# Kernel optimization log

Measured on AMD Instinct MI355X. Metric: run time of the kernel, lower is better.

The kernel has to match this reference:

```python
import jax, jax.numpy as jnp
import numpy as np

B, N, C, H, W = 16, 10, 128, 48, 48

def setup_inputs() -> dict:
    key = jax.random.key(0)
    k0, k1 = jax.random.split(key, 2)
    x = jax.random.normal(k0, (B, N, C, H, W), dtype=jnp.float32)
    # trainable interpolation params, initialized to 0.5 as in the torch module
    pos_dec = jnp.full((N,), 0.5, dtype=jnp.float32)
    length_dec = jnp.full((N,), 0.5, dtype=jnp.float32)
    # 1x1 conv == channel-mixing matmul over N*C channels
    NC = N * C
    conv_w = jax.random.normal(k1, (NC, NC), dtype=jnp.float32) * (1.0 / np.sqrt(NC))
    conv_b = jnp.zeros((NC,), dtype=jnp.float32)
    return {"x": x, "pos_dec": pos_dec, "length_dec": length_dec,
            "conv_w": conv_w, "conv_b": conv_b}


def reference(x, pos_dec, length_dec, conv_w, conv_b):
    b, n, c, h, w = x.shape
    d = c * h * w
    q = x.reshape(b, n, d)          # proj_query (B,N,CHW)
    k = q                           # proj_key has the same flattened features
    # bi_interpolate with pos_int=i, length_int=1 reduces in closed form to:
    #   s0 = (1-pd)*K[i]   + pd*K[i+1]                      (key_short row)
    #   s1 = ld*((1-pd)*K[i+1] + pd*K[i+2])                 (zero-padded short mixed with key_long)
    # where indices wrap mod N (key was concatenated with itself).
    idx = jnp.arange(n)
    k1_ = k[:, (idx + 1) % n]       # (B,N,D)
    k2_ = k[:, (idx + 2) % n]
    pd = pos_dec[None, :, None]
    ld = length_dec[None, :, None]
    s0 = (1.0 - pd) * k + pd * k1_
    s1 = ld * ((1.0 - pd) * k1_ + pd * k2_)
    S = jnp.stack([s0, s1], axis=2)                 # (B,N,2,D) interpolated keys per group
    logits = jnp.einsum('bnd,bnkd->bnk', q, S)      # per-group 2-way attention scores
    attn = jax.nn.softmax(logits, axis=-1)          # softmax over the 2 searched keys
    out = jnp.einsum('bnk,bnkd->bnd', attn, S)      # (B,N,D)
    feat = out.reshape(b, n * c, h, w)
    conv = jnp.einsum('oc,bchw->bohw', conv_w, feat) + conv_b[None, :, None, None]
    return conv + x.reshape(b, n * c, h, w)
```

## Files before the change

kernel.cpp:

```cpp
#include <hip/hip_runtime.h>
#include <hip/hip_bf16.h>

#define BB 16
#define NN 10
#define CC 128
#define HWD 2304
#define DD (CC*HWD)
#define NC (NN*CC)

#define CH2 72
#define CHUNK2 4096

#define BM 256
#define BN 128
#define BK 32
#define TK (NC/BK)

typedef __bf16 bf16x8 __attribute__((ext_vector_type(8)));
typedef float  f32x4  __attribute__((ext_vector_type(4)));

#define FEAT_BYTES ((size_t)BB*HWD*NC*2)
#define WB_BYTES   ((size_t)NC*NC*2)
#define PART_FLOATS (BB*NN*CH2*3)

__device__ __forceinline__ ushort f2bf(float f) {
    __hip_bfloat16 h = __float2bfloat16(f);
    return *reinterpret_cast<ushort*>(&h);
}

__device__ __forceinline__ void gload_lds16(const ushort* g, ushort* l) {
    __builtin_amdgcn_global_load_lds(
        (const __attribute__((address_space(1))) void*)(const void*)g,
        (__attribute__((address_space(3))) void*)(void*)l,
        16, 0, 0);
}

__global__ __launch_bounds__(256) void k_dots(const float* __restrict__ x,
                                              float* __restrict__ part) {
    int blk = blockIdx.x;
    int ch = blk % CH2;
    int b  = blk / CH2;
    const float* base = x + (size_t)b*NN*DD + (size_t)ch*CHUNK2;
    int t = threadIdx.x;

    float4 cur[4], nxt[4], inc[4];
    #pragma unroll
    for (int i = 0; i < 4; ++i) cur[i] = *(const float4*)(base + (size_t)0*DD + i*1024 + t*4);
    #pragma unroll
    for (int i = 0; i < 4; ++i) nxt[i] = *(const float4*)(base + (size_t)1*DD + i*1024 + t*4);

    __shared__ float red[4][3];
    int w = t >> 6, l = t & 63;

    for (int n = 0; n < NN; ++n) {
        int n2 = (n + 2) % NN;
        #pragma unroll
        for (int i = 0; i < 4; ++i) inc[i] = *(const float4*)(base + (size_t)n2*DD + i*1024 + t*4);

        float s0 = 0.f, s1 = 0.f, s2 = 0.f;
        #pragma unroll
        for (int i = 0; i < 4; ++i) {
            s0 += cur[i].x*cur[i].x + cur[i].y*cur[i].y + cur[i].z*cur[i].z + cur[i].w*cur[i].w;
            s1 += cur[i].x*nxt[i].x + cur[i].y*nxt[i].y + cur[i].z*nxt[i].z + cur[i].w*nxt[i].w;
            s2 += cur[i].x*inc[i].x + cur[i].y*inc[i].y + cur[i].z*inc[i].z + cur[i].w*inc[i].w;
        }
        for (int o = 32; o > 0; o >>= 1) {
            s0 += __shfl_down(s0, o);
            s1 += __shfl_down(s1, o);
            s2 += __shfl_down(s2, o);
        }
        if (l == 0) { red[w][0] = s0; red[w][1] = s1; red[w][2] = s2; }
        __syncthreads();
        if (t == 0) {
            float r0 = 0.f, r1 = 0.f, r2 = 0.f;
            #pragma unroll
            for (int i = 0; i < 4; ++i) { r0 += red[i][0]; r1 += red[i][1]; r2 += red[i][2]; }
            float* o = part + ((size_t)(b*NN + n)*CH2 + ch)*3;
            o[0] = r0; o[1] = r1; o[2] = r2;
        }
        __syncthreads();
        #pragma unroll
        for (int i = 0; i < 4; ++i) { cur[i] = nxt[i]; nxt[i] = inc[i]; }
    }
}

__global__ void k_coef(const float* __restrict__ part,
                       const float* __restrict__ pos_dec,
                       const float* __restrict__ len_dec,
                       float* __restrict__ coef) {
    int bn = threadIdx.x;
    if (bn >= BB*NN) return;
    int n = bn % NN;
    float d0 = 0.f, d1 = 0.f, d2 = 0.f;
    const float* p = part + (size_t)bn*CH2*3;
    for (int i = 0; i < CH2; ++i) { d0 += p[i*3]; d1 += p[i*3+1]; d2 += p[i*3+2]; }
    float pd = pos_dec[n], ld = len_dec[n];
    float l0 = (1.f - pd)*d0 + pd*d1;
    float l1 = ld*((1.f - pd)*d1 + pd*d2);
    float m  = fmaxf(l0, l1);
    float e0 = expf(l0 - m), e1 = expf(l1 - m);
    float inv = 1.f/(e0 + e1);
    float a0 = e0*inv, a1 = e1*inv;
    coef[bn*3+0] = a0*(1.f - pd);
    coef[bn*3+1] = a0*pd + a1*ld*(1.f - pd);
    coef[bn*3+2] = a1*ld*pd;
}

__global__ __launch_bounds__(256) void k_wconv(const float* __restrict__ w,
                                               ushort* __restrict__ wb) {
    int i = blockIdx.x*blockDim.x + threadIdx.x;
    size_t idx = (size_t)i*4;
    if (idx >= (size_t)NC*NC) return;
    float4 a = *(const float4*)(w + idx);
    ushort4 o;
    o.x = f2bf(a.x); o.y = f2bf(a.y); o.z = f2bf(a.z); o.w = f2bf(a.w);
    *(ushort4*)(wb + idx) = o;
}

__global__ __launch_bounds__(256) void k_feat(const float* __restrict__ x,
                                              const float* __restrict__ coef,
                                              ushort* __restrict__ featT) {
    __shared__ float tile[32*129];
    int hwt = blockIdx.x;
    int b   = blockIdx.y;
    int t = threadIdx.x;
    int hw0 = hwt*32;
    const float* xb = x + (size_t)b*NN*DD;

    int c_[4], ch_[4];
    size_t off_[4];
    #pragma unroll
    for (int i = 0; i < 4; ++i) {
        int s = i*256 + t;
        c_[i] = s >> 3; ch_[i] = s & 7;
        off_[i] = (size_t)c_[i]*HWD + hw0 + ch_[i]*4;
    }

    float4 s0[4], s1[4], s2[4], s3[4];
    #pragma unroll
    for (int i = 0; i < 4; ++i) s0[i] = *(const float4*)(xb + (size_t)0*DD + off_[i]);
    #pragma unroll
    for (int i = 0; i < 4; ++i) s1[i] = *(const float4*)(xb + (size_t)1*DD + off_[i]);
    #pragma unroll
    for (int i = 0; i < 4; ++i) s2[i] = *(const float4*)(xb + (size_t)2*DD + off_[i]);

    for (int n = 0; n < NN; ++n) {
        int n3 = (n + 3) % NN;
        #pragma unroll
        for (int i = 0; i < 4; ++i) s3[i] = *(const float4*)(xb + (size_t)n3*DD + off_[i]);

        int bn = b*NN + n;
        float c0 = coef[bn*3+0], c1 = coef[bn*3+1], c2 = coef[bn*3+2];

        #pragma unroll
        for (int i = 0; i < 4; ++i) {
            int hwb = ch_[i]*4, cc = c_[i];
            tile[(hwb+0)*129 + cc] = c0*s0[i].x + c1*s1[i].x + c2*s2[i].x;
            tile[(hwb+1)*129 + cc] = c0*s0[i].y + c1*s1[i].y + c2*s2[i].y;
            tile[(hwb+2)*129 + cc] = c0*s0[i].z + c1*s1[i].z + c2*s2[i].z;
            tile[(hwb+3)*129 + cc] = c0*s0[i].w + c1*s1[i].w + c2*s2[i].w;
        }
        __syncthreads();

        int hwl = t >> 4;
        int cc0 = (t & 15) * 8;
        #pragma unroll
        for (int p = 0; p < 2; ++p) {
            int hw = p*16 + hwl;
            const float* src = &tile[hw*129 + cc0];
            union { ushort us[8]; uint4 v; } pk;
            #pragma unroll
            for (int j = 0; j < 8; ++j) pk.us[j] = f2bf(src[j]);
            ushort* dst = featT + (size_t)b*HWD*NC + (size_t)(hw0 + hw)*NC + n*CC + cc0;
            *(uint4*)dst = pk.v;
        }
        __syncthreads();
        #pragma unroll
        for (int i = 0; i < 4; ++i) { s0[i] = s1[i]; s1[i] = s2[i]; s2[i] = s3[i]; }
    }
}

__global__ __launch_bounds__(512, 4) void k_gemm(const ushort* __restrict__ Wb,
                                                 const ushort* __restrict__ featT,
                                                 const float* __restrict__ bias,
                                                 const float* __restrict__ x,
                                                 float* __restrict__ out) {
    __shared__ ushort As[2][BM*BK];
    __shared__ ushort Bs[2][BN*BK];

    int bid = blockIdx.x;
    int wkid = (bid & 7) * 180 + (bid >> 3);
    int b    = wkid / 90;
    int rem  = wkid % 90;
    int hwt  = rem / 5;
    int ot   = rem % 5;
    int o0 = ot*BM, hw0 = hwt*BN;

    int t = threadIdx.x;
    int l = t & 63;
    int w = t >> 6;
    int wr = w >> 1, wc = w & 1;

    const ushort* Ag = Wb + (size_t)o0*NC;
    const ushort* Bg = featT + (size_t)b*HWD*NC + (size_t)hw0*NC;

    int r0 = t >> 2, c0 = t & 3;
    size_t g0 = (size_t)r0*NC + (size_t)((c0 ^ ((r0 >> 1) & 3)) * 8);

#define STAGE(buf_, kt_) do { \
    size_t k0_ = (size_t)(kt_)*BK; \
    ushort* da_ = &As[buf_][0]; \
    ushort* db_ = &Bs[buf_][0]; \
    gload_lds16(Ag + g0 + k0_,                  da_ + t*8); \
    gload_lds16(Ag + g0 + (size_t)128*NC + k0_, da_ + (512 + t)*8); \
    gload_lds16(Bg + g0 + k0_,                  db_ + t*8); \
} while (0)

    int fr = l & 15;
    int fc = l >> 4;

    f32x4 acc[4][4] = {};

    STAGE(0, 0);
    __syncthreads();

    for (int kt = 0; kt < TK; ++kt) {
        int buf = kt & 1;
        if (kt + 1 < TK) STAGE(buf ^ 1, kt + 1);
        __builtin_amdgcn_sched_barrier(0);

        const ushort* as = &As[buf][0];
        const ushort* bs = &Bs[buf][0];

        bf16x8 afr[4], bfr[4];
        #pragma unroll
        for (int m = 0; m < 4; ++m) {
            int row = wr*64 + m*16 + fr;
            afr[m] = *(const bf16x8*)&as[row*BK + ((fc ^ ((row >> 1) & 3))*8)];
        }
        #pragma unroll
        for (int n = 0; n < 4; ++n) {
            int row = wc*64 + n*16 + fr;
            bfr[n] = *(const bf16x8*)&bs[row*BK + ((fc ^ ((row >> 1) & 3))*8)];
        }
        #pragma unroll
        for (int m = 0; m < 4; ++m)
            #pragma unroll
            for (int n = 0; n < 4; ++n)
                acc[m][n] = __builtin_amdgcn_mfma_f32_16x16x32_bf16(afr[m], bfr[n], acc[m][n], 0, 0, 0);

        __syncthreads();
    }
#undef STAGE

    #pragma unroll
    for (int m = 0; m < 4; ++m) {
        int ro_base = o0 + wr*64 + m*16 + ((l >> 4) << 2);
        #pragma unroll
        for (int n = 0; n < 4; ++n) {
            int col = hw0 + wc*64 + n*16 + (l & 15);
            #pragma unroll
            for (int r = 0; r < 4; ++r) {
                int ro = ro_base + r;
                size_t idx = (size_t)b*NC*HWD + (size_t)ro*HWD + col;
                out[idx] = acc[m][n][r] + bias[ro] + x[idx];
            }
        }
    }
}

extern "C" void kernel_launch(void* const* d_in, const int* in_sizes, int n_in,
                              void* d_out, int out_size, void* d_ws, size_t ws_size,
                              hipStream_t stream) {
    const float* x       = (const float*)d_in[0];
    const float* pos_dec = (const float*)d_in[1];
    const float* len_dec = (const float*)d_in[2];
    const float* conv_w  = (const float*)d_in[3];
    const float* conv_b  = (const float*)d_in[4];
    float* out = (float*)d_out;

    char* ws = (char*)d_ws;
    ushort* featT = (ushort*)ws;
    ushort* wb    = (ushort*)(ws + FEAT_BYTES);
    float*  part  = (float*)(ws + FEAT_BYTES + WB_BYTES);
    float*  coef  = part + PART_FLOATS;

    k_dots <<<dim3(BB*CH2), 256, 0, stream>>>(x, part);
    k_coef <<<dim3(1), 256, 0, stream>>>(part, pos_dec, len_dec, coef);
    k_wconv<<<dim3(1600), 256, 0, stream>>>(conv_w, wb);
    k_feat <<<dim3(72, BB), 256, 0, stream>>>(x, coef, featT);
    k_gemm <<<dim3(1440), 512, 0, stream>>>(wb, featT, conv_b, x, out);
}
```

Baseline: 305.8 us.

## Enlarge GEMM tile to 256x256x64 with finely interleaved LDS/MFMA pipeline

The GEMM tile grows from 256x128 with K=32 to 256x256 with K=64, which halves the block count. Each K step is split into four 32-wide sub-tiles whose global-to-LDS loads are issued between MFMA phases, using explicit barriers, waitcnt and setprio. The larger tile raises operand reuse and cuts global and LDS traffic per FLOP. In exchange it holds more accumulator registers and runs at lower occupancy (launch bounds 2), with only 720 blocks to fill the CUs.

Measured after the change: 300.2 us. Within noise of the previous version (-1.8%).

```diff
diff --git a/kernel.cpp b/kernel.cpp
--- a/kernel.cpp
+++ b/kernel.cpp
@@ -12,8 +12,8 @@
 #define CHUNK2 4096
 
 #define BM 256
-#define BN 128
-#define BK 32
+#define BN 256
+#define BK 64
 #define TK (NC/BK)
 
 typedef __bf16 bf16x8 __attribute__((ext_vector_type(8)));
@@ -180,82 +180,170 @@
     }
 }
 
-__global__ __launch_bounds__(512, 4) void k_gemm(const ushort* __restrict__ Wb,
+#define BAR()   __builtin_amdgcn_s_barrier()
+#define SB()    __builtin_amdgcn_sched_barrier(0)
+#define LGKM0() asm volatile("s_waitcnt lgkmcnt(0)" ::: "memory")
+#define VM(N)   asm volatile("s_waitcnt vmcnt(" #N ")" ::: "memory")
+
+__global__ __launch_bounds__(512, 2) void k_gemm(const ushort* __restrict__ Wb,
                                                  const ushort* __restrict__ featT,
                                                  const float* __restrict__ bias,
                                                  const float* __restrict__ x,
                                                  float* __restrict__ out) {
-    __shared__ ushort As[2][BM*BK];
-    __shared__ ushort Bs[2][BN*BK];
+    __shared__ ushort L[2][4][BM*32];
 
     int bid = blockIdx.x;
-    int wkid = (bid & 7) * 180 + (bid >> 3);
-    int b    = wkid / 90;
-    int rem  = wkid % 90;
-    int hwt  = rem / 5;
-    int ot   = rem % 5;
+    int wkid = (bid & 7) * 90 + (bid >> 3);
+    int b   = wkid / 45;
+    int r45 = wkid % 45;
+    int hwt = r45 / 5;
+    int ot  = r45 % 5;
     int o0 = ot*BM, hw0 = hwt*BN;
 
     int t = threadIdx.x;
     int l = t & 63;
     int w = t >> 6;
-    int wr = w >> 1, wc = w & 1;
+    int wr = w >> 2, wc = w & 3;
 
     const ushort* Ag = Wb + (size_t)o0*NC;
     const ushort* Bg = featT + (size_t)b*HWD*NC + (size_t)hw0*NC;
 
     int r0 = t >> 2, c0 = t & 3;
     size_t g0 = (size_t)r0*NC + (size_t)((c0 ^ ((r0 >> 1) & 3)) * 8);
-
-#define STAGE(buf_, kt_) do { \
-    size_t k0_ = (size_t)(kt_)*BK; \
-    ushort* da_ = &As[buf_][0]; \
-    ushort* db_ = &Bs[buf_][0]; \
-    gload_lds16(Ag + g0 + k0_,                  da_ + t*8); \
-    gload_lds16(Ag + g0 + (size_t)128*NC + k0_, da_ + (512 + t)*8); \
-    gload_lds16(Bg + g0 + k0_,                  db_ + t*8); \
-} while (0)
+    size_t g1 = g0 + (size_t)128*NC;
+
+#define STAGE(nb_, reg_, gp_) do { \
+    gload_lds16((gp_) + g0, &L[nb_][reg_][t*8]); \
+    gload_lds16((gp_) + g1, &L[nb_][reg_][(512 + t)*8]); } while (0)
 
     int fr = l & 15;
-    int fc = l >> 4;
-
-    f32x4 acc[4][4] = {};
-
-    STAGE(0, 0);
-    __syncthreads();
-
-    for (int kt = 0; kt < TK; ++kt) {
-        int buf = kt & 1;
-        if (kt + 1 < TK) STAGE(buf ^ 1, kt + 1);
-        __builtin_amdgcn_sched_barrier(0);
-
-        const ushort* as = &As[buf][0];
-        const ushort* bs = &Bs[buf][0];
-
-        bf16x8 afr[4], bfr[4];
-        #pragma unroll
-        for (int m = 0; m < 4; ++m) {
-            int row = wr*64 + m*16 + fr;
-            afr[m] = *(const bf16x8*)&as[row*BK + ((fc ^ ((row >> 1) & 3))*8)];
-        }
-        #pragma unroll
-        for (int n = 0; n < 4; ++n) {
-            int row = wc*64 + n*16 + fr;
-            bfr[n] = *(const bf16x8*)&bs[row*BK + ((fc ^ ((row >> 1) & 3))*8)];
-        }
-        #pragma unroll
-        for (int m = 0; m < 4; ++m)
-            #pragma unroll
-            for (int n = 0; n < 4; ++n)
-                acc[m][n] = __builtin_amdgcn_mfma_f32_16x16x32_bf16(afr[m], bfr[n], acc[m][n], 0, 0, 0);
-
-        __syncthreads();
+    int kc = ((l >> 4) ^ ((l >> 1) & 3)) * 8;
+    int rowA = (wr*128 + fr)*32 + kc;
+    int rowB = (wc*64  + fr)*32 + kc;
+
+    f32x4 acc[8][4] = {};
+    bf16x8 af[8], bfA, bfB;
+
+    STAGE(0, 0, Ag);
+    STAGE(0, 2, Bg);
+    STAGE(0, 1, Ag + 32);
+    STAGE(0, 3, Bg + 32);
+    VM(4);
+    BAR(); SB();
+
+    for (int kt = 0; kt < TK - 1; ++kt) {
+        int buf = kt & 1, nbuf = buf ^ 1;
+        const ushort* A0 = &L[buf][0][0];
+        const ushort* A1 = &L[buf][1][0];
+        const ushort* B0 = &L[buf][2][0];
+        const ushort* B1 = &L[buf][3][0];
+        const ushort* Agk = Ag + (size_t)(kt + 1)*BK;
+        const ushort* Bgk = Bg + (size_t)(kt + 1)*BK;
+
+        #pragma unroll
+        for (int i = 0; i < 8; ++i) af[i] = *(const bf16x8*)&A0[rowA + i*512];
+        bfA = *(const bf16x8*)&B0[rowB];
+        bfB = *(const bf16x8*)&B0[rowB + 512];
+        STAGE(nbuf, 0, Agk);
+        SB(); BAR(); LGKM0(); SB();
+        __builtin_amdgcn_s_setprio(1);
+        #pragma unroll
+        for (int i = 0; i < 8; ++i) {
+            acc[i][0] = __builtin_amdgcn_mfma_f32_16x16x32_bf16(af[i], bfA, acc[i][0], 0, 0, 0);
+            acc[i][1] = __builtin_amdgcn_mfma_f32_16x16x32_bf16(af[i], bfB, acc[i][1], 0, 0, 0);
+        }
+        __builtin_amdgcn_s_setprio(0);
+        SB(); BAR(); SB();
+
+        bfA = *(const bf16x8*)&B0[rowB + 2*512];
+        bfB = *(const bf16x8*)&B0[rowB + 3*512];
+        STAGE(nbuf, 2, Bgk);
+        SB(); BAR(); LGKM0(); SB();
+        __builtin_amdgcn_s_setprio(1);
+        #pragma unroll
+        for (int i = 0; i < 8; ++i) {
+            acc[i][2] = __builtin_amdgcn_mfma_f32_16x16x32_bf16(af[i], bfA, acc[i][2], 0, 0, 0);
+            acc[i][3] = __builtin_amdgcn_mfma_f32_16x16x32_bf16(af[i], bfB, acc[i][3], 0, 0, 0);
+        }
+        __builtin_amdgcn_s_setprio(0);
+        SB(); VM(4); BAR(); SB();
+
+        #pragma unroll
+        for (int i = 0; i < 8; ++i) af[i] = *(const bf16x8*)&A1[rowA + i*512];
+        bfA = *(const bf16x8*)&B1[rowB];
+        bfB = *(const bf16x8*)&B1[rowB + 512];
+        STAGE(nbuf, 1, Agk + 32);
+        SB(); BAR(); LGKM0(); SB();
+        __builtin_amdgcn_s_setprio(1);
+        #pragma unroll
+        for (int i = 0; i < 8; ++i) {
+            acc[i][0] = __builtin_amdgcn_mfma_f32_16x16x32_bf16(af[i], bfA, acc[i][0], 0, 0, 0);
+            acc[i][1] = __builtin_amdgcn_mfma_f32_16x16x32_bf16(af[i], bfB, acc[i][1], 0, 0, 0);
+        }
+        __builtin_amdgcn_s_setprio(0);
+        SB(); BAR(); SB();
+
+        bfA = *(const bf16x8*)&B1[rowB + 2*512];
+        bfB = *(const bf16x8*)&B1[rowB + 3*512];
+        STAGE(nbuf, 3, Bgk + 32);
+        SB(); BAR(); LGKM0(); SB();
+        __builtin_amdgcn_s_setprio(1);
+        #pragma unroll
+        for (int i = 0; i < 8; ++i) {
+            acc[i][2] = __builtin_amdgcn_mfma_f32_16x16x32_bf16(af[i], bfA, acc[i][2], 0, 0, 0);
+            acc[i][3] = __builtin_amdgcn_mfma_f32_16x16x32_bf16(af[i], bfB, acc[i][3], 0, 0, 0);
+        }
+        __builtin_amdgcn_s_setprio(0);
+        SB(); VM(4); BAR(); SB();
+    }
+
+    {
+        const int buf = (TK - 1) & 1;
+        const ushort* A0 = &L[buf][0][0];
+        const ushort* A1 = &L[buf][1][0];
+        const ushort* B0 = &L[buf][2][0];
+        const ushort* B1 = &L[buf][3][0];
+
+        #pragma unroll
+        for (int i = 0; i < 8; ++i) af[i] = *(const bf16x8*)&A0[rowA + i*512];
+        bfA = *(const bf16x8*)&B0[rowB];
+        bfB = *(const bf16x8*)&B0[rowB + 512];
+        #pragma unroll
+        for (int i = 0; i < 8; ++i) {
+            acc[i][0] = __builtin_amdgcn_mfma_f32_16x16x32_bf16(af[i], bfA, acc[i][0], 0, 0, 0);
+            acc[i][1] = __builtin_amdgcn_mfma_f32_16x16x32_bf16(af[i], bfB, acc[i][1], 0, 0, 0);
+        }
+        bfA = *(const bf16x8*)&B0[rowB + 2*512];
+        bfB = *(const bf16x8*)&B0[rowB + 3*512];
+        #pragma unroll
+        for (int i = 0; i < 8; ++i) {
+            acc[i][2] = __builtin_amdgcn_mfma_f32_16x16x32_bf16(af[i], bfA, acc[i][2], 0, 0, 0);
+            acc[i][3] = __builtin_amdgcn_mfma_f32_16x16x32_bf16(af[i], bfB, acc[i][3], 0, 0, 0);
+        }
+        VM(0);
+        BAR(); SB();
+        #pragma unroll
+        for (int i = 0; i < 8; ++i) af[i] = *(const bf16x8*)&A1[rowA + i*512];
+        bfA = *(const bf16x8*)&B1[rowB];
+        bfB = *(const bf16x8*)&B1[rowB + 512];
+        #pragma unroll
+        for (int i = 0; i < 8; ++i) {
+            acc[i][0] = __builtin_amdgcn_mfma_f32_16x16x32_bf16(af[i], bfA, acc[i][0], 0, 0, 0);
+            acc[i][1] = __builtin_amdgcn_mfma_f32_16x16x32_bf16(af[i], bfB, acc[i][1], 0, 0, 0);
+        }
+        bfA = *(const bf16x8*)&B1[rowB + 2*512];
+        bfB = *(const bf16x8*)&B1[rowB + 3*512];
+        #pragma unroll
+        for (int i = 0; i < 8; ++i) {
+            acc[i][2] = __builtin_amdgcn_mfma_f32_16x16x32_bf16(af[i], bfA, acc[i][2], 0, 0, 0);
+            acc[i][3] = __builtin_amdgcn_mfma_f32_16x16x32_bf16(af[i], bfB, acc[i][3], 0, 0, 0);
+        }
     }
 #undef STAGE
 
     #pragma unroll
-    for (int m = 0; m < 4; ++m) {
-        int ro_base = o0 + wr*64 + m*16 + ((l >> 4) << 2);
+    for (int m = 0; m < 8; ++m) {
+        int ro_base = o0 + wr*128 + m*16 + ((l >> 4) << 2);
         #pragma unroll
         for (int n = 0; n < 4; ++n) {
             int col = hw0 + wc*64 + n*16 + (l & 15);
@@ -289,5 +377,5 @@
     k_coef <<<dim3(1), 256, 0, stream>>>(part, pos_dec, len_dec, coef);
     k_wconv<<<dim3(1600), 256, 0, stream>>>(conv_w, wb);
     k_feat <<<dim3(72, BB), 256, 0, stream>>>(x, coef, featT);
-    k_gemm <<<dim3(1440), 512, 0, stream>>>(wb, featT, conv_b, x, out);
-}
+    k_gemm <<<dim3(720), 512, 0, stream>>>(wb, featT, conv_b, x, out);
+}
```
